# Optimization experiments

Hardware: AMD Instinct MI355X
Metric: run time of the kernel (lower is better)

Reference implementation:

```python
import jax, jax.numpy as jnp
import numpy as np

N, L, H = 64, 1024, 1024

def setup_inputs() -> dict:
    key = jax.random.key(0)
    ks = jax.random.split(key, 6)
    scale = 1.0 / np.sqrt(H)
    return {
        "decoder_hidden": jax.random.normal(ks[0], (N, H), dtype=jnp.float32),
        "encoder_hiddens": jax.random.normal(ks[1], (N, L, H), dtype=jnp.float32),
        "mask": jax.random.randint(ks[2], (N, L), 0, 2) > 0,  # True = PAD position
        "W_h": jax.random.normal(ks[3], (H, H), dtype=jnp.float32) * scale,
        "W_s": jax.random.normal(ks[4], (H, H), dtype=jnp.float32) * scale,
        "v": jax.random.normal(ks[5], (H,), dtype=jnp.float32) * scale,
    }

def reference(decoder_hidden, encoder_hiddens, mask, W_h, W_s, v):
    # score(h_t, h_s) = v^T tanh(W_h h_t + W_s h_s)
    # torch Linear: y = x @ W.T
    dh = decoder_hidden @ W_h.T                      # [N, H]
    eh = jnp.einsum('nlh,kh->nlk', encoder_hiddens, W_s)  # [N, L, H]
    score = jnp.tanh(dh[:, None, :] + eh) @ v        # [N, L]
    score = jnp.where(mask, -jnp.inf, score)
    attn_weights = jax.nn.softmax(score, axis=1)     # [N, L]
    context = jnp.einsum('nl,nlh->nh', attn_weights, encoder_hiddens)  # [N, H]
    return (context, attn_weights)
```

## Files before the change

### kernel.cpp

```cpp
#include <hip/hip_runtime.h>
#include <hip/hip_bf16.h>
#include <math.h>

#define N_  64
#define L_  1024
#define H_  1024
#define NL_ (N_ * L_)
#define NT_ 16

typedef __attribute__((ext_vector_type(8))) short bf16x8;
typedef __attribute__((ext_vector_type(4))) float f32x4;
typedef unsigned short ushort_t;
typedef unsigned int uint_t;

__device__ inline ushort_t f32_to_bf16_rne(float f) {
    uint_t u = __float_as_uint(f);
    u += 0x7FFFu + ((u >> 16) & 1u);
    return (ushort_t)(u >> 16);
}

__global__ __launch_bounds__(256) void convert_bf16_kernel(const float* __restrict__ src,
                                                           ushort_t* __restrict__ dst,
                                                           size_t nvec8) {
    size_t stride = (size_t)gridDim.x * 256;
    for (size_t g = (size_t)blockIdx.x * 256 + threadIdx.x; g < nvec8; g += stride) {
        size_t i = g * 8;
        float4 a = *(const float4*)(src + i);
        float4 b = *(const float4*)(src + i + 4);
        union { bf16x8 v; ushort_t u[8]; } o;
        o.u[0] = f32_to_bf16_rne(a.x); o.u[1] = f32_to_bf16_rne(a.y);
        o.u[2] = f32_to_bf16_rne(a.z); o.u[3] = f32_to_bf16_rne(a.w);
        o.u[4] = f32_to_bf16_rne(b.x); o.u[5] = f32_to_bf16_rne(b.y);
        o.u[6] = f32_to_bf16_rne(b.z); o.u[7] = f32_to_bf16_rne(b.w);
        *(bf16x8*)(dst + i) = o.v;
    }
}

__global__ __launch_bounds__(256) void dh_kernel(const float* __restrict__ ddec,
                                                 const float* __restrict__ Wh,
                                                 float* __restrict__ dh) {
    int i = blockIdx.x * 256 + threadIdx.x;
    int n = i >> 10;
    const float* a = ddec + (size_t)n * H_;
    const float* w = Wh + (size_t)(i & (H_ - 1)) * H_;
    float acc = 0.f;
#pragma unroll 8
    for (int h = 0; h < H_; h += 4) {
        float4 av = *(const float4*)(a + h);
        float4 wv = *(const float4*)(w + h);
        acc += av.x * wv.x + av.y * wv.y + av.z * wv.z + av.w * wv.w;
    }
    dh[i] = acc;
}

__device__ __forceinline__ void glds(const ushort_t* g, ushort_t* l) {
    __builtin_amdgcn_global_load_lds((const __attribute__((address_space(1))) void*)g,
                                     (__attribute__((address_space(3))) void*)l,
                                     16, 0, 0);
}

__global__ __launch_bounds__(512, 2) void score_mfma_kernel(const ushort_t* __restrict__ enc_bf,
                                                            const ushort_t* __restrict__ ws_bf,
                                                            const float* __restrict__ dh,
                                                            const float* __restrict__ v,
                                                            float* __restrict__ score) {
    __shared__ ushort_t lds[65536];

    const int b  = blockIdx.x;
    const int i0 = ((b & 7) | ((b >> 5) << 3)) << 8;
    const int k0 = ((b >> 3) & 3) << 8;
    const int tid  = threadIdx.x;
    const int lane = tid & 63;
    const int w    = tid >> 6;
    const int wr   = (w >> 2) << 7;
    const int wc   = (w & 3) << 6;
    const int m    = lane & 15;
    const int q    = lane >> 4;
    const int half = w >> 2;
    const int grp  = w & 3;

    const int g_lane = (lane >> 3) * H_ + (((lane & 7) ^ (lane >> 3)) << 3);
    const int csw0 = ((q ^ (m & 7)) << 3);
    const int csw1 = (((4 | q) ^ (m & 7)) << 3);

    const int rA0 = (half << 7) + (grp << 5);
    const int rB0 = (grp << 6) + (half << 4);

    {
        const ushort_t* gA = enc_bf + (size_t)i0 * H_ + g_lane;
        const ushort_t* gB = ws_bf  + (size_t)k0 * H_ + g_lane;
        ushort_t* An = lds;
        ushort_t* Bn = lds + 32768;
        glds(gA + (size_t)(rA0 +  0) * H_, An + (rA0 +  0) * 64);
        glds(gA + (size_t)(rA0 +  8) * H_, An + (rA0 +  8) * 64);
        glds(gA + (size_t)(rA0 + 16) * H_, An + (rA0 + 16) * 64);
        glds(gA + (size_t)(rA0 + 24) * H_, An + (rA0 + 24) * 64);
        glds(gB + (size_t)(rB0 +  0) * H_, Bn + (rB0 +  0) * 64);
        glds(gB + (size_t)(rB0 +  8) * H_, Bn + (rB0 +  8) * 64);
        glds(gB + (size_t)(rB0 + 32) * H_, Bn + (rB0 + 32) * 64);
        glds(gB + (size_t)(rB0 + 40) * H_, Bn + (rB0 + 40) * 64);
        asm volatile("s_waitcnt vmcnt(0)" ::: "memory");
        __builtin_amdgcn_s_barrier();
    }

    f32x4 acc[8][4];
#pragma unroll
    for (int a = 0; a < 8; a++)
#pragma unroll
        for (int c = 0; c < 4; c++)
            acc[a][c] = (f32x4){0.f, 0.f, 0.f, 0.f};

    const int rowA = wr + m;
    const int rowB = wc + m;

#pragma unroll 2
    for (int kt = 0; kt < NT_; ++kt) {
        ushort_t* Ac = lds + ((kt & 1) << 14);
        ushort_t* Bc = lds + 32768 + ((kt & 1) << 14);
        ushort_t* An = lds + (((kt + 1) & 1) << 14);
        ushort_t* Bn = lds + 32768 + (((kt + 1) & 1) << 14);
        const int h0n = ((kt + 1) & (NT_ - 1)) << 6;
        const ushort_t* gA = enc_bf + (size_t)i0 * H_ + h0n + g_lane;
        const ushort_t* gB = ws_bf  + (size_t)k0 * H_ + h0n + g_lane;

        bf16x8 af[8], b0, b1, b2, b3;

#pragma unroll
        for (int ti = 0; ti < 8; ti++)
            af[ti] = *(const bf16x8*)(Ac + (rowA + ti * 16) * 64 + csw0);
        b0 = *(const bf16x8*)(Bc + (rowB +  0) * 64 + csw0);
        b1 = *(const bf16x8*)(Bc + (rowB + 16) * 64 + csw0);
        glds(gA + (size_t)(rA0 + 0) * H_, An + (rA0 + 0) * 64);
        glds(gA + (size_t)(rA0 + 8) * H_, An + (rA0 + 8) * 64);
        __builtin_amdgcn_s_barrier();
        asm volatile("s_waitcnt lgkmcnt(0)" ::: "memory");
        __builtin_amdgcn_sched_barrier(0);
        __builtin_amdgcn_s_setprio(1);
#pragma unroll
        for (int ti = 0; ti < 8; ti++)
            acc[ti][0] = __builtin_amdgcn_mfma_f32_16x16x32_bf16(af[ti], b0, acc[ti][0], 0, 0, 0);
#pragma unroll
        for (int ti = 0; ti < 8; ti++)
            acc[ti][1] = __builtin_amdgcn_mfma_f32_16x16x32_bf16(af[ti], b1, acc[ti][1], 0, 0, 0);
        __builtin_amdgcn_s_setprio(0);
        asm volatile("s_waitcnt vmcnt(2)" ::: "memory");
        __builtin_amdgcn_s_barrier();

        b2 = *(const bf16x8*)(Bc + (rowB + 32) * 64 + csw0);
        b3 = *(const bf16x8*)(Bc + (rowB + 48) * 64 + csw0);
        glds(gA + (size_t)(rA0 + 16) * H_, An + (rA0 + 16) * 64);
        glds(gA + (size_t)(rA0 + 24) * H_, An + (rA0 + 24) * 64);
        __builtin_amdgcn_s_barrier();
        asm volatile("s_waitcnt lgkmcnt(0)" ::: "memory");
        __builtin_amdgcn_sched_barrier(0);
        __builtin_amdgcn_s_setprio(1);
#pragma unroll
        for (int ti = 0; ti < 8; ti++)
            acc[ti][2] = __builtin_amdgcn_mfma_f32_16x16x32_bf16(af[ti], b2, acc[ti][2], 0, 0, 0);
#pragma unroll
        for (int ti = 0; ti < 8; ti++)
            acc[ti][3] = __builtin_amdgcn_mfma_f32_16x16x32_bf16(af[ti], b3, acc[ti][3], 0, 0, 0);
        __builtin_amdgcn_s_setprio(0);
        __builtin_amdgcn_s_barrier();

#pragma unroll
        for (int ti = 0; ti < 8; ti++)
            af[ti] = *(const bf16x8*)(Ac + (rowA + ti * 16) * 64 + csw1);
        b0 = *(const bf16x8*)(Bc + (rowB +  0) * 64 + csw1);
        b1 = *(const bf16x8*)(Bc + (rowB + 16) * 64 + csw1);
        glds(gB + (size_t)(rB0 + 0) * H_, Bn + (rB0 + 0) * 64);
        glds(gB + (size_t)(rB0 + 8) * H_, Bn + (rB0 + 8) * 64);
        __builtin_amdgcn_s_barrier();
        asm volatile("s_waitcnt lgkmcnt(0)" ::: "memory");
        __builtin_amdgcn_sched_barrier(0);
        __builtin_amdgcn_s_setprio(1);
#pragma unroll
        for (int ti = 0; ti < 8; ti++)
            acc[ti][0] = __builtin_amdgcn_mfma_f32_16x16x32_bf16(af[ti], b0, acc[ti][0], 0, 0, 0);
#pragma unroll
        for (int ti = 0; ti < 8; ti++)
            acc[ti][1] = __builtin_amdgcn_mfma_f32_16x16x32_bf16(af[ti], b1, acc[ti][1], 0, 0, 0);
        __builtin_amdgcn_s_setprio(0);
        __builtin_amdgcn_s_barrier();

        b2 = *(const bf16x8*)(Bc + (rowB + 32) * 64 + csw1);
        b3 = *(const bf16x8*)(Bc + (rowB + 48) * 64 + csw1);
        glds(gB + (size_t)(rB0 + 32) * H_, Bn + (rB0 + 32) * 64);
        glds(gB + (size_t)(rB0 + 40) * H_, Bn + (rB0 + 40) * 64);
        __builtin_amdgcn_s_barrier();
        asm volatile("s_waitcnt lgkmcnt(0)" ::: "memory");
        __builtin_amdgcn_sched_barrier(0);
        __builtin_amdgcn_s_setprio(1);
#pragma unroll
        for (int ti = 0; ti < 8; ti++)
            acc[ti][2] = __builtin_amdgcn_mfma_f32_16x16x32_bf16(af[ti], b2, acc[ti][2], 0, 0, 0);
#pragma unroll
        for (int ti = 0; ti < 8; ti++)
            acc[ti][3] = __builtin_amdgcn_mfma_f32_16x16x32_bf16(af[ti], b3, acc[ti][3], 0, 0, 0);
        __builtin_amdgcn_s_setprio(0);
        asm volatile("s_waitcnt vmcnt(2)" ::: "memory");
        __builtin_amdgcn_s_barrier();
    }

    const int nb = i0 >> 10;
    float vv[4], dhv[4];
#pragma unroll
    for (int tj = 0; tj < 4; tj++) {
        int k = k0 + wc + tj * 16 + m;
        vv[tj]  = v[k];
        dhv[tj] = dh[nb * H_ + k];
    }
#pragma unroll
    for (int ti = 0; ti < 8; ti++) {
#pragma unroll
        for (int reg = 0; reg < 4; reg++) {
            float s = 0.f;
#pragma unroll
            for (int tj = 0; tj < 4; tj++) {
                float x  = dhv[tj] + acc[ti][tj][reg];
                float e2 = __expf(2.f * x);
                s += vv[tj] * (1.f - 2.f / (e2 + 1.f));
            }
            s += __shfl_xor(s, 1);
            s += __shfl_xor(s, 2);
            s += __shfl_xor(s, 4);
            s += __shfl_xor(s, 8);
            if (m == 0) {
                int i_local = wr + ti * 16 + q * 4 + reg;
                atomicAdd(&score[i0 + i_local], s);
            }
        }
    }
}

__global__ __launch_bounds__(256) void softmax_kernel(const float* __restrict__ score,
                                                      const int* __restrict__ mask,
                                                      float* __restrict__ attn) {
    const int n = blockIdx.x;
    const int t = threadIdx.x;
    __shared__ float redmax[4];
    __shared__ float redsum[4];

    float s[4];
    int   mk[4];
    float mymax = -INFINITY;
#pragma unroll
    for (int j = 0; j < 4; j++) {
        int l = t + j * 256;
        mk[j] = mask[n * L_ + l];
        s[j] = mk[j] ? -INFINITY : score[n * L_ + l];
        mymax = fmaxf(mymax, s[j]);
    }
#pragma unroll
    for (int off = 1; off < 64; off <<= 1)
        mymax = fmaxf(mymax, __shfl_xor(mymax, off));
    if ((t & 63) == 0) redmax[t >> 6] = mymax;
    __syncthreads();
    float gmax = fmaxf(fmaxf(redmax[0], redmax[1]), fmaxf(redmax[2], redmax[3]));

    float e[4];
    float mysum = 0.f;
#pragma unroll
    for (int j = 0; j < 4; j++) {
        e[j] = mk[j] ? 0.f : __expf(s[j] - gmax);
        mysum += e[j];
    }
#pragma unroll
    for (int off = 1; off < 64; off <<= 1)
        mysum += __shfl_xor(mysum, off);
    if ((t & 63) == 0) redsum[t >> 6] = mysum;
    __syncthreads();
    float gsum = redsum[0] + redsum[1] + redsum[2] + redsum[3];
    float inv = 1.f / gsum;
#pragma unroll
    for (int j = 0; j < 4; j++)
        attn[n * L_ + t + j * 256] = e[j] * inv;
}

__global__ __launch_bounds__(128) void context_partial_kernel(const ushort_t* __restrict__ enc_bf,
                                                              const float* __restrict__ attn,
                                                              float* __restrict__ cpart) {
    const int n  = blockIdx.x;
    const int lc = blockIdx.y;
    const int l0 = lc * 128;
    const int t  = threadIdx.x;
    const int h0 = t * 8;

    __shared__ float w[128];
    w[t] = attn[n * L_ + l0 + t];
    __syncthreads();

    const ushort_t* base = enc_bf + (size_t)n * L_ * H_ + (size_t)l0 * H_ + h0;
    float acc[8] = {};
#pragma unroll 4
    for (int l = 0; l < 128; l++) {
        union { bf16x8 v; ushort_t u[8]; } e;
        e.v = *(const bf16x8*)(base + (size_t)l * H_);
        float wl = w[l];
#pragma unroll
        for (int j = 0; j < 8; j++)
            acc[j] += wl * __uint_as_float(((uint_t)e.u[j]) << 16);
    }
    float* dst = cpart + ((size_t)lc * N_ + n) * H_ + h0;
    *(float4*)(dst + 0) = (float4){acc[0], acc[1], acc[2], acc[3]};
    *(float4*)(dst + 4) = (float4){acc[4], acc[5], acc[6], acc[7]};
}

__global__ __launch_bounds__(256) void context_reduce_kernel(const float* __restrict__ cpart,
                                                             float* __restrict__ ctx) {
    int i = blockIdx.x * 256 + threadIdx.x;
    float s = 0.f;
#pragma unroll
    for (int lc = 0; lc < 8; lc++)
        s += cpart[(size_t)lc * N_ * H_ + i];
    ctx[i] = s;
}

extern "C" void kernel_launch(void* const* d_in, const int* in_sizes, int n_in,
                              void* d_out, int out_size, void* d_ws, size_t ws_size,
                              hipStream_t stream) {
    const float* ddec = (const float*)d_in[0];
    const float* enc  = (const float*)d_in[1];
    const int*   mask = (const int*)d_in[2];
    const float* Wh   = (const float*)d_in[3];
    const float* Ws   = (const float*)d_in[4];
    const float* v    = (const float*)d_in[5];

    float* out_ctx  = (float*)d_out;
    float* out_attn = out_ctx + N_ * H_;

    ushort_t* enc_bf = (ushort_t*)d_ws;
    ushort_t* ws_bf  = enc_bf + (size_t)NL_ * H_;
    float*    dh     = (float*)(ws_bf + (size_t)H_ * H_);
    float*    score  = dh + N_ * H_;
    float*    cpart  = score + NL_;

    convert_bf16_kernel<<<4096, 256, 0, stream>>>(enc, enc_bf, (size_t)NL_ * H_ / 8);
    convert_bf16_kernel<<<512, 256, 0, stream>>>(Ws, ws_bf, (size_t)H_ * H_ / 8);

    hipMemsetAsync(score, 0, (size_t)NL_ * sizeof(float), stream);

    dh_kernel<<<NL_ / 256, 256, 0, stream>>>(ddec, Wh, dh);

    score_mfma_kernel<<<1024, 512, 0, stream>>>(enc_bf, ws_bf, dh, v, score);

    softmax_kernel<<<N_, 256, 0, stream>>>(score, mask, out_attn);

    dim3 g4(N_, 8);
    context_partial_kernel<<<g4, 128, 0, stream>>>(enc_bf, out_attn, cpart);
    context_reduce_kernel<<<NL_ / 1024 * 4, 256, 0, stream>>>(cpart, out_ctx);
}
```

Baseline: 607.0 us.

## Restructure score GEMM main loop into two-phase register double-buffered pipeline

Replaces the four-barrier-per-half-tile schedule with two phases per K tile. Each phase issues all global-to-LDS copies up front and runs MFMAs on fragments already held in registers, while the LDS reads for the next half-tile stay in flight under a partial lgkmcnt wait. Per-wave copy rows become one contiguous slice (w*32) for both A and B. The aim is fewer barriers and better overlap of LDS reads and global loads with MFMA work, at the cost of doubling the fragment registers, which may pressure the occupancy of 2 workgroups per CU.

```diff
diff --git a/kernel.cpp b/kernel.cpp
--- a/kernel.cpp
+++ b/kernel.cpp
@@ -76,29 +76,26 @@
     const int wc   = (w & 3) << 6;
     const int m    = lane & 15;
     const int q    = lane >> 4;
-    const int half = w >> 2;
-    const int grp  = w & 3;
 
     const int g_lane = (lane >> 3) * H_ + (((lane & 7) ^ (lane >> 3)) << 3);
     const int csw0 = ((q ^ (m & 7)) << 3);
     const int csw1 = (((4 | q) ^ (m & 7)) << 3);
 
-    const int rA0 = (half << 7) + (grp << 5);
-    const int rB0 = (grp << 6) + (half << 4);
+    const int rS = w << 5;
+    const int rowA = wr + m;
+    const int rowB = wc + m;
+
+    const ushort_t* gAb = enc_bf + (size_t)(i0 + rS) * H_ + g_lane;
+    const ushort_t* gBb = ws_bf  + (size_t)(k0 + rS) * H_ + g_lane;
 
     {
-        const ushort_t* gA = enc_bf + (size_t)i0 * H_ + g_lane;
-        const ushort_t* gB = ws_bf  + (size_t)k0 * H_ + g_lane;
         ushort_t* An = lds;
         ushort_t* Bn = lds + 32768;
-        glds(gA + (size_t)(rA0 +  0) * H_, An + (rA0 +  0) * 64);
-        glds(gA + (size_t)(rA0 +  8) * H_, An + (rA0 +  8) * 64);
-        glds(gA + (size_t)(rA0 + 16) * H_, An + (rA0 + 16) * 64);
-        glds(gA + (size_t)(rA0 + 24) * H_, An + (rA0 + 24) * 64);
-        glds(gB + (size_t)(rB0 +  0) * H_, Bn + (rB0 +  0) * 64);
-        glds(gB + (size_t)(rB0 +  8) * H_, Bn + (rB0 +  8) * 64);
-        glds(gB + (size_t)(rB0 + 32) * H_, Bn + (rB0 + 32) * 64);
-        glds(gB + (size_t)(rB0 + 40) * H_, Bn + (rB0 + 40) * 64);
+#pragma unroll
+        for (int j = 0; j < 4; j++) {
+            glds(gAb + (size_t)(j * 8) * H_, An + (rS + j * 8) * 64);
+            glds(gBb + (size_t)(j * 8) * H_, Bn + (rS + j * 8) * 64);
+        }
         asm volatile("s_waitcnt vmcnt(0)" ::: "memory");
         __builtin_amdgcn_s_barrier();
     }
@@ -110,95 +107,68 @@
         for (int c = 0; c < 4; c++)
             acc[a][c] = (f32x4){0.f, 0.f, 0.f, 0.f};
 
-    const int rowA = wr + m;
-    const int rowB = wc + m;
-
-#pragma unroll 2
+    bf16x8 aA[8], bA[4];
+    bf16x8 aB[8], bB[4];
+
+    {
+        const ushort_t* Ac = lds;
+        const ushort_t* Bc = lds + 32768;
+#pragma unroll
+        for (int ti = 0; ti < 8; ti++)
+            aA[ti] = *(const bf16x8*)(Ac + (rowA + ti * 16) * 64 + csw0);
+#pragma unroll
+        for (int tj = 0; tj < 4; tj++)
+            bA[tj] = *(const bf16x8*)(Bc + (rowB + tj * 16) * 64 + csw0);
+    }
+
     for (int kt = 0; kt < NT_; ++kt) {
         ushort_t* Ac = lds + ((kt & 1) << 14);
         ushort_t* Bc = lds + 32768 + ((kt & 1) << 14);
         ushort_t* An = lds + (((kt + 1) & 1) << 14);
         ushort_t* Bn = lds + 32768 + (((kt + 1) & 1) << 14);
-        const int h0n = ((kt + 1) & (NT_ - 1)) << 6;
-        const ushort_t* gA = enc_bf + (size_t)i0 * H_ + h0n + g_lane;
-        const ushort_t* gB = ws_bf  + (size_t)k0 * H_ + h0n + g_lane;
-
-        bf16x8 af[8], b0, b1, b2, b3;
-
+        const size_t hoff = (size_t)(((kt + 1) & (NT_ - 1)) << 6);
+
+#pragma unroll
+        for (int j = 0; j < 4; j++) {
+            glds(gAb + hoff + (size_t)(j * 8) * H_, An + (rS + j * 8) * 64);
+            glds(gBb + hoff + (size_t)(j * 8) * H_, Bn + (rS + j * 8) * 64);
+        }
 #pragma unroll
         for (int ti = 0; ti < 8; ti++)
-            af[ti] = *(const bf16x8*)(Ac + (rowA + ti * 16) * 64 + csw0);
-        b0 = *(const bf16x8*)(Bc + (rowB +  0) * 64 + csw0);
-        b1 = *(const bf16x8*)(Bc + (rowB + 16) * 64 + csw0);
-        glds(gA + (size_t)(rA0 + 0) * H_, An + (rA0 + 0) * 64);
-        glds(gA + (size_t)(rA0 + 8) * H_, An + (rA0 + 8) * 64);
-        __builtin_amdgcn_s_barrier();
-        asm volatile("s_waitcnt lgkmcnt(0)" ::: "memory");
+            aB[ti] = *(const bf16x8*)(Ac + (rowA + ti * 16) * 64 + csw1);
+#pragma unroll
+        for (int tj = 0; tj < 4; tj++)
+            bB[tj] = *(const bf16x8*)(Bc + (rowB + tj * 16) * 64 + csw1);
+        asm volatile("s_waitcnt lgkmcnt(12)" ::: "memory");
         __builtin_amdgcn_sched_barrier(0);
         __builtin_amdgcn_s_setprio(1);
 #pragma unroll
+        for (int tj = 0; tj < 4; tj++)
+#pragma unroll
+            for (int ti = 0; ti < 8; ti++)
+                acc[ti][tj] = __builtin_amdgcn_mfma_f32_16x16x32_bf16(
+                    aA[ti], bA[tj], acc[ti][tj], 0, 0, 0);
+        __builtin_amdgcn_s_setprio(0);
+        __builtin_amdgcn_sched_barrier(0);
+        asm volatile("s_waitcnt vmcnt(0)" ::: "memory");
+        __builtin_amdgcn_s_barrier();
+
+#pragma unroll
         for (int ti = 0; ti < 8; ti++)
-            acc[ti][0] = __builtin_amdgcn_mfma_f32_16x16x32_bf16(af[ti], b0, acc[ti][0], 0, 0, 0);
-#pragma unroll
-        for (int ti = 0; ti < 8; ti++)
-            acc[ti][1] = __builtin_amdgcn_mfma_f32_16x16x32_bf16(af[ti], b1, acc[ti][1], 0, 0, 0);
-        __builtin_amdgcn_s_setprio(0);
-        asm volatile("s_waitcnt vmcnt(2)" ::: "memory");
-        __builtin_amdgcn_s_barrier();
-
-        b2 = *(const bf16x8*)(Bc + (rowB + 32) * 64 + csw0);
-        b3 = *(const bf16x8*)(Bc + (rowB + 48) * 64 + csw0);
-        glds(gA + (size_t)(rA0 + 16) * H_, An + (rA0 + 16) * 64);
-        glds(gA + (size_t)(rA0 + 24) * H_, An + (rA0 + 24) * 64);
-        __builtin_amdgcn_s_barrier();
-        asm volatile("s_waitcnt lgkmcnt(0)" ::: "memory");
+            aA[ti] = *(const bf16x8*)(An + (rowA + ti * 16) * 64 + csw0);
+#pragma unroll
+        for (int tj = 0; tj < 4; tj++)
+            bA[tj] = *(const bf16x8*)(Bn + (rowB + tj * 16) * 64 + csw0);
+        asm volatile("s_waitcnt lgkmcnt(12)" ::: "memory");
         __builtin_amdgcn_sched_barrier(0);
         __builtin_amdgcn_s_setprio(1);
 #pragma unroll
-        for (int ti = 0; ti < 8; ti++)
-            acc[ti][2] = __builtin_amdgcn_mfma_f32_16x16x32_bf16(af[ti], b2, acc[ti][2], 0, 0, 0);
-#pragma unroll
-        for (int ti = 0; ti < 8; ti++)
-            acc[ti][3] = __builtin_amdgcn_mfma_f32_16x16x32_bf16(af[ti], b3, acc[ti][3], 0, 0, 0);
+        for (int tj = 0; tj < 4; tj++)
+#pragma unroll
+            for (int ti = 0; ti < 8; ti++)
+                acc[ti][tj] = __builtin_amdgcn_mfma_f32_16x16x32_bf16(
+                    aB[ti], bB[tj], acc[ti][tj], 0, 0, 0);
         __builtin_amdgcn_s_setprio(0);
-        __builtin_amdgcn_s_barrier();
-
-#pragma unroll
-        for (int ti = 0; ti < 8; ti++)
-            af[ti] = *(const bf16x8*)(Ac + (rowA + ti * 16) * 64 + csw1);
-        b0 = *(const bf16x8*)(Bc + (rowB +  0) * 64 + csw1);
-        b1 = *(const bf16x8*)(Bc + (rowB + 16) * 64 + csw1);
-        glds(gB + (size_t)(rB0 + 0) * H_, Bn + (rB0 + 0) * 64);
-        glds(gB + (size_t)(rB0 + 8) * H_, Bn + (rB0 + 8) * 64);
-        __builtin_amdgcn_s_barrier();
-        asm volatile("s_waitcnt lgkmcnt(0)" ::: "memory");
-        __builtin_amdgcn_sched_barrier(0);
-        __builtin_amdgcn_s_setprio(1);
-#pragma unroll
-        for (int ti = 0; ti < 8; ti++)
-            acc[ti][0] = __builtin_amdgcn_mfma_f32_16x16x32_bf16(af[ti], b0, acc[ti][0], 0, 0, 0);
-#pragma unroll
-        for (int ti = 0; ti < 8; ti++)
-            acc[ti][1] = __builtin_amdgcn_mfma_f32_16x16x32_bf16(af[ti], b1, acc[ti][1], 0, 0, 0);
-        __builtin_amdgcn_s_setprio(0);
-        __builtin_amdgcn_s_barrier();
-
-        b2 = *(const bf16x8*)(Bc + (rowB + 32) * 64 + csw1);
-        b3 = *(const bf16x8*)(Bc + (rowB + 48) * 64 + csw1);
-        glds(gB + (size_t)(rB0 + 32) * H_, Bn + (rB0 + 32) * 64);
-        glds(gB + (size_t)(rB0 + 40) * H_, Bn + (rB0 + 40) * 64);
-        __builtin_amdgcn_s_barrier();
-        asm volatile("s_waitcnt lgkmcnt(0)" ::: "memory");
-        __builtin_amdgcn_sched_barrier(0);
-        __builtin_amdgcn_s_setprio(1);
-#pragma unroll
-        for (int ti = 0; ti < 8; ti++)
-            acc[ti][2] = __builtin_amdgcn_mfma_f32_16x16x32_bf16(af[ti], b2, acc[ti][2], 0, 0, 0);
-#pragma unroll
-        for (int ti = 0; ti < 8; ti++)
-            acc[ti][3] = __builtin_amdgcn_mfma_f32_16x16x32_bf16(af[ti], b3, acc[ti][3], 0, 0, 0);
-        __builtin_amdgcn_s_setprio(0);
-        asm volatile("s_waitcnt vmcnt(2)" ::: "memory");
         __builtin_amdgcn_s_barrier();
     }
 
```

After: 636.1 us. +4.8%, slower.
